# Kernel tuning notes

Measured on AMD Instinct MI355X. Metric: run time of the kernel, lower is better.

Reference implementation:

```python
import jax, jax.numpy as jnp
import numpy as np

B, SEQ, C, H, OVERLAP, G, K, D = 16, 8192, 192, 16, 4, 6, 1024, 8
FIX = H * C                      # 3072 (proj_ratio = 1.0, no in/out proj)
DG = (FIX * OVERLAP) // G        # 2048, per-group dim
W = SEQ // H                     # 512 time frames
T = W // OVERLAP                 # 128 grouped frames


def _l2norm(x, eps=1e-12):
    return x / jnp.clip(jnp.linalg.norm(x, axis=-1, keepdims=True), eps)


def setup_inputs() -> dict:
    key = jax.random.key(0)
    k0, k1, k2, k3 = jax.random.split(key, 4)
    z = jax.random.normal(k0, (B, SEQ, C), jnp.float32)
    # stacked per-group parameters (all groups have equal dim DG)
    proj_down = jax.random.normal(k1, (G, DG, D), jnp.float32) * (DG ** -0.5)
    proj_up = jax.random.normal(k2, (G, D, DG), jnp.float32) * (D ** -0.5)
    codebooks = jax.random.normal(k3, (G, K, D), jnp.float32)
    return {"z": z, "proj_down": proj_down, "proj_up": proj_up, "codebooks": codebooks}


def reference(z, proj_down, proj_up, codebooks):
    # --- pre_process: 'b (h w) c -> b w (c h)' then fold overlap ---
    zz = z.reshape(B, H, W, C)                      # b h w c
    zz = jnp.transpose(zz, (0, 2, 3, 1))            # b w c h
    zz = zz.reshape(B, W, FIX)                      # b w (c h)
    zz = zz.reshape(B, T, OVERLAP * FIX)            # fold overlap frames
    zg = zz.reshape(B, T, G, DG)                    # split into G groups

    # --- per-group codebook VQ (vectorized over G) ---
    z_e = jnp.einsum('btgd,gde->btge', zg, proj_down)           # (B,T,G,D)
    sim = jnp.einsum('btge,gke->btgk', _l2norm(z_e), _l2norm(codebooks))
    code = jnp.argmax(sim, axis=-1)                             # (B,T,G)
    gidx = jnp.arange(G)[None, None, :]
    z_q = codebooks[gidx, code]                                 # (B,T,G,D)

    # per-batch-element losses, mean over (T, D) per group, averaged over groups
    commitment = jnp.mean((z_e - jax.lax.stop_gradient(z_q)) ** 2, axis=(1, 3)).mean(axis=1)
    codebook_l = jnp.mean((jax.lax.stop_gradient(z_e) - z_q) ** 2, axis=(1, 3)).mean(axis=1)

    # straight-through estimator + up projection
    z_q_st = z_e + jax.lax.stop_gradient(z_q - z_e)
    z_up = jnp.einsum('btge,ged->btgd', z_q_st, proj_up)        # (B,T,G,DG)
    z_up = z_up.reshape(B, T, OVERLAP * FIX)

    # --- post_process: unfold overlap, 'b w (c h) -> b (h w) c' ---
    out = z_up.reshape(B, W, FIX)                   # b w (c h)
    out = out.reshape(B, W, C, H)
    out = jnp.transpose(out, (0, 3, 1, 2))          # b h w c
    out = out.reshape(B, SEQ, C)
    return out, commitment, codebook_l
```

## Files before the change

### kernel.cpp

```cpp
#include <hip/hip_runtime.h>
#include <math.h>

#define B_ 16
#define SEQ_ 8192
#define C_ 192
#define H_ 16
#define OV_ 4
#define G_ 6
#define K_ 1024
#define D_ 8
#define DG_ 2048
#define W_ 512
#define T_ 128
#define TT 4
#define OUT_ELEMS (B_ * SEQ_ * C_)



__global__ __launch_bounds__(256) void vq_prep(
    const float* __restrict__ pd, const float* __restrict__ pu,
    const float* __restrict__ cb,
    float* __restrict__ pd_p, float* __restrict__ pu_p,
    double* __restrict__ cbn, float* __restrict__ loss_slots)
{
  int i = blockIdx.x * 256 + threadIdx.x;
  if (i < 98304) {
    int e = i & 7, dp = (i >> 3) & 2047, g = i >> 14;
    int h = dp >> 7, ul = dp & 127, d = (ul << 4) + h;
    pd_p[i] = pd[(g << 14) + (d << 3) + e];
  } else if (i < 196608) {
    int i2 = i - 98304;
    int dp = i2 & 2047, e = (i2 >> 11) & 7, g = i2 >> 14;
    int h = dp >> 7, ul = dp & 127, d = (ul << 4) + h;
    pu_p[i2] = pu[(g << 14) + (e << 11) + d];
  } else if (i < 202752) {
    int j = i - 196608;
    const float* row = cb + (j << 3);
    double ss = 0.0;
    #pragma unroll
    for (int e = 0; e < 8; ++e) { double x = (double)row[e]; ss += x * x; }
    double inv = 1.0 / fmax(sqrt(ss), 1e-12);
    #pragma unroll
    for (int e = 0; e < 8; ++e) cbn[(j << 3) + e] = (double)row[e] * inv;
  } else if (i < 202784) {
    loss_slots[i - 202752] = 0.0f;
  }
}

__global__ __launch_bounds__(256) void vq_main(
    const float* __restrict__ z, const float* __restrict__ cb,
    const float* __restrict__ pd_p, const float* __restrict__ pu_p,
    const double* __restrict__ cbn,
    float* __restrict__ out, float* __restrict__ loss_slots)
{
  __shared__ __align__(16) float zs[TT * DG_];
  __shared__ double ze_d[TT * 8];
  __shared__ float  zq_s[TT * 8];
  __shared__ double wr_s[4][TT];
  __shared__ int    wr_k[4][TT];
  __shared__ float  lossv[TT];

  const int tid = threadIdx.x;
  const int tc  = blockIdx.x;
  const int g   = blockIdx.y;
  const int b   = blockIdx.z;

  const float* zb = z + (size_t)b * (SEQ_ * C_);

  #pragma unroll
  for (int t = 0; t < TT; ++t) {
    int wbase = (tc * TT + t) * OV_;
    #pragma unroll
    for (int j = 0; j < 2; ++j) {
      int v  = j * 256 + tid;
      int h  = v >> 5;
      int ul = (v & 31) << 2;
      int u  = (g << 7) + ul;
      int o  = (u * 683) >> 17;
      int c  = u - o * 192;
      const float4 val = *(const float4*)(zb + (h * 512 + wbase + o) * 192 + c);
      *(float4*)(&zs[t * DG_ + (h << 7) + ul]) = val;
    }
  }
  __syncthreads();

  double acc[TT][8];
  #pragma unroll
  for (int t = 0; t < TT; ++t)
    #pragma unroll
    for (int e = 0; e < 8; ++e) acc[t][e] = 0.0;

  #pragma unroll
  for (int i = 0; i < 8; ++i) {
    int dp = i * 256 + tid;
    const float4 p0 = *(const float4*)(pd_p + ((((g << 11) + dp) << 3)));
    const float4 p1 = *(const float4*)(pd_p + ((((g << 11) + dp) << 3) + 4));
    #pragma unroll
    for (int t = 0; t < TT; ++t) {
      double zv = (double)zs[t * DG_ + dp];
      acc[t][0] = fma(zv, (double)p0.x, acc[t][0]);
      acc[t][1] = fma(zv, (double)p0.y, acc[t][1]);
      acc[t][2] = fma(zv, (double)p0.z, acc[t][2]);
      acc[t][3] = fma(zv, (double)p0.w, acc[t][3]);
      acc[t][4] = fma(zv, (double)p1.x, acc[t][4]);
      acc[t][5] = fma(zv, (double)p1.y, acc[t][5]);
      acc[t][6] = fma(zv, (double)p1.z, acc[t][6]);
      acc[t][7] = fma(zv, (double)p1.w, acc[t][7]);
    }
  }

  double* part_d = (double*)zs;
  #pragma unroll
  for (int r = 0; r < 2; ++r) {
    __syncthreads();
    #pragma unroll
    for (int kkl = 0; kkl < 16; ++kkl) {
      int kk = r * 16 + kkl;
      part_d[kkl * 256 + tid] = acc[kk >> 3][kk & 7];
    }
    __syncthreads();
    int kkl = tid >> 4, jj = tid & 15;
    double partial = 0.0;
    #pragma unroll
    for (int s = 0; s < 16; ++s) {
      int p = (s + tid) & 15;
      partial += part_d[kkl * 256 + jj * 16 + p];
    }
    partial += __shfl_down(partial, 8);
    partial += __shfl_down(partial, 4);
    partial += __shfl_down(partial, 2);
    partial += __shfl_down(partial, 1);
    if (jj == 0) ze_d[r * 16 + kkl] = partial;
  }
  __syncthreads();

  double cd[4][8];
  #pragma unroll
  for (int q = 0; q < 4; ++q) {
    const double* cr = cbn + (((g << 10) + (q << 8) + tid) << 3);
    #pragma unroll
    for (int e = 0; e < 8; ++e) cd[q][e] = cr[e];
  }
  double bs[TT]; int bk[TT];
  #pragma unroll
  for (int t = 0; t < TT; ++t) {
    double zr[8];
    #pragma unroll
    for (int e = 0; e < 8; ++e) zr[e] = ze_d[t * 8 + e];
    bs[t] = -1.0e300; bk[t] = 0x7fffffff;
    #pragma unroll
    for (int q = 0; q < 4; ++q) {
      double s = 0.0;
      #pragma unroll
      for (int e = 0; e < 8; ++e) s = fma(zr[e], cd[q][e], s);
      int k = (q << 8) + tid;
      if (s > bs[t]) { bs[t] = s; bk[t] = k; }
    }
  }
  #pragma unroll
  for (int m = 32; m >= 1; m >>= 1) {
    #pragma unroll
    for (int t = 0; t < TT; ++t) {
      double os = __shfl_xor(bs[t], m);
      int    ok = __shfl_xor(bk[t], m);
      if (os > bs[t] || (os == bs[t] && ok < bk[t])) { bs[t] = os; bk[t] = ok; }
    }
  }
  int wv = tid >> 6;
  if ((tid & 63) == 0) {
    #pragma unroll
    for (int t = 0; t < TT; ++t) { wr_s[wv][t] = bs[t]; wr_k[wv][t] = bk[t]; }
  }
  __syncthreads();
  if (tid < TT) {
    int t = tid;
    double s0 = wr_s[0][t]; int k0 = wr_k[0][t];
    #pragma unroll
    for (int w2 = 1; w2 < 4; ++w2) {
      double s1 = wr_s[w2][t]; int k1 = wr_k[w2][t];
      if (s1 > s0 || (s1 == s0 && k1 < k0)) { s0 = s1; k0 = k1; }
    }
    const float* crow = cb + (((g << 10) + k0) << 3);
    double l = 0.0;
    #pragma unroll
    for (int e = 0; e < 8; ++e) {
      float qv = crow[e];
      zq_s[t * 8 + e] = qv;
      double dd = ze_d[t * 8 + e] - (double)qv;
      l = fma(dd, dd, l);
    }
    lossv[t] = (float)l;
  }
  __syncthreads();
  if (tid == 0) {
    float l = (lossv[0] + lossv[1] + lossv[2] + lossv[3]) * (1.0f / (T_ * D_ * G_));
    atomicAdd(loss_slots + b, l);
    atomicAdd(loss_slots + 16 + b, l);
  }

  float zqr[TT][8];
  #pragma unroll
  for (int t = 0; t < TT; ++t)
    #pragma unroll
    for (int e = 0; e < 8; ++e) zqr[t][e] = zq_s[t * 8 + e];

  #pragma unroll
  for (int j = 0; j < 8; ++j) {
    int dp = j * 256 + tid;
    int h = dp >> 7, ul = dp & 127;
    int u = (g << 7) + ul;
    int o = (u * 683) >> 17;
    int c = u - o * 192;
    float pv[8];
    #pragma unroll
    for (int e = 0; e < 8; ++e) pv[e] = pu_p[(g << 14) + (e << 11) + dp];
    size_t base = ((size_t)(b * SEQ_) + h * 512 + tc * (TT * OV_) + o) * 192 + c;
    #pragma unroll
    for (int t = 0; t < TT; ++t) {
      float v = 0.f;
      #pragma unroll
      for (int e = 0; e < 8; ++e) v = fmaf(zqr[t][e], pv[e], v);
      out[base + (size_t)(t * OV_ * 192)] = v;
    }
  }
}

extern "C" void kernel_launch(void* const* d_in, const int* in_sizes, int n_in,
                              void* d_out, int out_size, void* d_ws, size_t ws_size,
                              hipStream_t stream)
{
  const float* z  = (const float*)d_in[0];
  const float* pd = (const float*)d_in[1];
  const float* pu = (const float*)d_in[2];
  const float* cb = (const float*)d_in[3];
  float* out = (float*)d_out;
  float* loss_slots = out + OUT_ELEMS;

  float*  pd_p = (float*)d_ws;
  float*  pu_p = pd_p + 98304;
  double* cbn  = (double*)(pu_p + 98304);

  vq_prep<<<793, 256, 0, stream>>>(pd, pu, cb, pd_p, pu_p, cbn, loss_slots);
  dim3 grid(T_ / TT, G_, B_);
  vq_main<<<grid, 256, 0, stream>>>(z, cb, pd_p, pu_p, cbn, out, loss_slots);
}
```

Before: 212.4 us.

## Compute down-projection per wavefront directly from global memory, dropping shared staging

The down-projection no longer stages four time frames of z (32 KB) in shared memory followed by a two-pass shared-memory reduction. Each wavefront now owns one time frame, reads z and proj_down straight from global memory, and reduces its eight accumulators with xor shuffles. This cuts the per-block LDS footprint and several barriers, and a launch-bounds hint of 6 blocks per CU is added to raise occupancy. In exchange, each block reads proj_down four times instead of once, relying on cache, and the z reads become strided float2 loads rather than float4.

```diff
diff --git a/kernel.cpp b/kernel.cpp
--- a/kernel.cpp
+++ b/kernel.cpp
@@ -47,90 +47,72 @@
   }
 }
 
-__global__ __launch_bounds__(256) void vq_main(
+__global__ __launch_bounds__(256, 6) void vq_main(
     const float* __restrict__ z, const float* __restrict__ cb,
     const float* __restrict__ pd_p, const float* __restrict__ pu_p,
     const double* __restrict__ cbn,
     float* __restrict__ out, float* __restrict__ loss_slots)
 {
-  __shared__ __align__(16) float zs[TT * DG_];
   __shared__ double ze_d[TT * 8];
   __shared__ float  zq_s[TT * 8];
   __shared__ double wr_s[4][TT];
   __shared__ int    wr_k[4][TT];
   __shared__ float  lossv[TT];
 
-  const int tid = threadIdx.x;
-  const int tc  = blockIdx.x;
-  const int g   = blockIdx.y;
-  const int b   = blockIdx.z;
+  const int tid  = threadIdx.x;
+  const int lane = tid & 63;
+  const int wv   = tid >> 6;
+  const int tc   = blockIdx.x;
+  const int g    = blockIdx.y;
+  const int b    = blockIdx.z;
 
   const float* zb = z + (size_t)b * (SEQ_ * C_);
 
-  #pragma unroll
-  for (int t = 0; t < TT; ++t) {
-    int wbase = (tc * TT + t) * OV_;
-    #pragma unroll
-    for (int j = 0; j < 2; ++j) {
-      int v  = j * 256 + tid;
-      int h  = v >> 5;
-      int ul = (v & 31) << 2;
-      int u  = (g << 7) + ul;
-      int o  = (u * 683) >> 17;
-      int c  = u - o * 192;
-      const float4 val = *(const float4*)(zb + (h * 512 + wbase + o) * 192 + c);
-      *(float4*)(&zs[t * DG_ + (h << 7) + ul]) = val;
-    }
-  }
-  __syncthreads();
-
-  double acc[TT][8];
-  #pragma unroll
-  for (int t = 0; t < TT; ++t)
-    #pragma unroll
-    for (int e = 0; e < 8; ++e) acc[t][e] = 0.0;
-
-  #pragma unroll
-  for (int i = 0; i < 8; ++i) {
-    int dp = i * 256 + tid;
-    const float4 p0 = *(const float4*)(pd_p + ((((g << 11) + dp) << 3)));
-    const float4 p1 = *(const float4*)(pd_p + ((((g << 11) + dp) << 3) + 4));
-    #pragma unroll
-    for (int t = 0; t < TT; ++t) {
-      double zv = (double)zs[t * DG_ + dp];
-      acc[t][0] = fma(zv, (double)p0.x, acc[t][0]);
-      acc[t][1] = fma(zv, (double)p0.y, acc[t][1]);
-      acc[t][2] = fma(zv, (double)p0.z, acc[t][2]);
-      acc[t][3] = fma(zv, (double)p0.w, acc[t][3]);
-      acc[t][4] = fma(zv, (double)p1.x, acc[t][4]);
-      acc[t][5] = fma(zv, (double)p1.y, acc[t][5]);
-      acc[t][6] = fma(zv, (double)p1.z, acc[t][6]);
-      acc[t][7] = fma(zv, (double)p1.w, acc[t][7]);
-    }
-  }
-
-  double* part_d = (double*)zs;
-  #pragma unroll
-  for (int r = 0; r < 2; ++r) {
-    __syncthreads();
-    #pragma unroll
-    for (int kkl = 0; kkl < 16; ++kkl) {
-      int kk = r * 16 + kkl;
-      part_d[kkl * 256 + tid] = acc[kk >> 3][kk & 7];
-    }
-    __syncthreads();
-    int kkl = tid >> 4, jj = tid & 15;
-    double partial = 0.0;
-    #pragma unroll
-    for (int s = 0; s < 16; ++s) {
-      int p = (s + tid) & 15;
-      partial += part_d[kkl * 256 + jj * 16 + p];
-    }
-    partial += __shfl_down(partial, 8);
-    partial += __shfl_down(partial, 4);
-    partial += __shfl_down(partial, 2);
-    partial += __shfl_down(partial, 1);
-    if (jj == 0) ze_d[r * 16 + kkl] = partial;
+  {
+    const int wbase = (tc * TT + wv) * OV_;
+    const float* zcol = zb + (size_t)wbase * 192 + (g << 7) + (lane << 1);
+    const float4* pdg = (const float4*)(pd_p + ((g << 11) << 3));
+
+    double acc[8];
+    #pragma unroll
+    for (int e = 0; e < 8; ++e) acc[e] = 0.0;
+
+    #pragma unroll 2
+    for (int h = 0; h < 16; ++h) {
+      const float2 zv = *(const float2*)(zcol + h * (512 * 192));
+      const int dp = (h << 7) + (lane << 1);
+      const float4 p00 = pdg[(dp << 1) + 0];
+      const float4 p01 = pdg[(dp << 1) + 1];
+      const float4 p10 = pdg[(dp << 1) + 2];
+      const float4 p11 = pdg[(dp << 1) + 3];
+      const double z0 = (double)zv.x, z1 = (double)zv.y;
+      acc[0] = fma(z0, (double)p00.x, acc[0]);
+      acc[1] = fma(z0, (double)p00.y, acc[1]);
+      acc[2] = fma(z0, (double)p00.z, acc[2]);
+      acc[3] = fma(z0, (double)p00.w, acc[3]);
+      acc[4] = fma(z0, (double)p01.x, acc[4]);
+      acc[5] = fma(z0, (double)p01.y, acc[5]);
+      acc[6] = fma(z0, (double)p01.z, acc[6]);
+      acc[7] = fma(z0, (double)p01.w, acc[7]);
+      acc[0] = fma(z1, (double)p10.x, acc[0]);
+      acc[1] = fma(z1, (double)p10.y, acc[1]);
+      acc[2] = fma(z1, (double)p10.z, acc[2]);
+      acc[3] = fma(z1, (double)p10.w, acc[3]);
+      acc[4] = fma(z1, (double)p11.x, acc[4]);
+      acc[5] = fma(z1, (double)p11.y, acc[5]);
+      acc[6] = fma(z1, (double)p11.z, acc[6]);
+      acc[7] = fma(z1, (double)p11.w, acc[7]);
+    }
+
+    #pragma unroll
+    for (int m = 32; m >= 1; m >>= 1) {
+      #pragma unroll
+      for (int e = 0; e < 8; ++e) acc[e] += __shfl_xor(acc[e], m);
+    }
+    if (lane == 0) {
+      #pragma unroll
+      for (int e = 0; e < 8; ++e) ze_d[wv * 8 + e] = acc[e];
+    }
   }
   __syncthreads();
 
@@ -166,10 +148,10 @@
       if (os > bs[t] || (os == bs[t] && ok < bk[t])) { bs[t] = os; bk[t] = ok; }
     }
   }
-  int wv = tid >> 6;
+  int wv4 = tid >> 6;
   if ((tid & 63) == 0) {
     #pragma unroll
-    for (int t = 0; t < TT; ++t) { wr_s[wv][t] = bs[t]; wr_k[wv][t] = bk[t]; }
+    for (int t = 0; t < TT; ++t) { wr_s[wv4][t] = bs[t]; wr_k[wv4][t] = bk[t]; }
   }
   __syncthreads();
   if (tid < TT) {
```

Result: slower. 372.2 us (+75.3%).

## Stream z directly from global into projection, split output dims across half-blocks

Applied to the files above, without the earlier changes.

The down-projection no longer stages a 32 KB tile of z in shared memory. Each thread now reads float2 pairs of z straight from global memory, and the two halves of the block each handle 4 of the 8 output dims. This halves the register accumulators and shrinks shared memory to a small reduction buffer, and launch bounds now request 6 blocks per CU. The aim is higher occupancy and no LDS staging or barrier cost. The codebook scoring loop is also reorganised to load two codebook rows at a time, which lowers register pressure. The trade-off is less coalesced global loads of z, which are 8-byte strided per thread, and each z element is now read twice, once by each half-block.

```diff
diff --git a/kernel.cpp b/kernel.cpp
--- a/kernel.cpp
+++ b/kernel.cpp
@@ -47,13 +47,13 @@
   }
 }
 
-__global__ __launch_bounds__(256) void vq_main(
+__global__ __launch_bounds__(256, 6) void vq_main(
     const float* __restrict__ z, const float* __restrict__ cb,
     const float* __restrict__ pd_p, const float* __restrict__ pu_p,
     const double* __restrict__ cbn,
     float* __restrict__ out, float* __restrict__ loss_slots)
 {
-  __shared__ __align__(16) float zs[TT * DG_];
+  __shared__ double part_d[16 * 128];
   __shared__ double ze_d[TT * 8];
   __shared__ float  zq_s[TT * 8];
   __shared__ double wr_s[4][TT];
@@ -61,100 +61,100 @@
   __shared__ float  lossv[TT];
 
   const int tid = threadIdx.x;
+  const int tl  = tid & 127;
+  const int eh  = tid >> 7;
   const int tc  = blockIdx.x;
   const int g   = blockIdx.y;
   const int b   = blockIdx.z;
 
   const float* zb = z + (size_t)b * (SEQ_ * C_);
 
-  #pragma unroll
-  for (int t = 0; t < TT; ++t) {
-    int wbase = (tc * TT + t) * OV_;
-    #pragma unroll
-    for (int j = 0; j < 2; ++j) {
-      int v  = j * 256 + tid;
-      int h  = v >> 5;
-      int ul = (v & 31) << 2;
-      int u  = (g << 7) + ul;
-      int o  = (u * 683) >> 17;
-      int c  = u - o * 192;
-      const float4 val = *(const float4*)(zb + (h * 512 + wbase + o) * 192 + c);
-      *(float4*)(&zs[t * DG_ + (h << 7) + ul]) = val;
-    }
-  }
-  __syncthreads();
-
-  double acc[TT][8];
+  double acc[TT][4];
   #pragma unroll
   for (int t = 0; t < TT; ++t)
     #pragma unroll
-    for (int e = 0; e < 8; ++e) acc[t][e] = 0.0;
-
-  #pragma unroll
-  for (int i = 0; i < 8; ++i) {
-    int dp = i * 256 + tid;
-    const float4 p0 = *(const float4*)(pd_p + ((((g << 11) + dp) << 3)));
-    const float4 p1 = *(const float4*)(pd_p + ((((g << 11) + dp) << 3) + 4));
-    #pragma unroll
-    for (int t = 0; t < TT; ++t) {
-      double zv = (double)zs[t * DG_ + dp];
-      acc[t][0] = fma(zv, (double)p0.x, acc[t][0]);
-      acc[t][1] = fma(zv, (double)p0.y, acc[t][1]);
-      acc[t][2] = fma(zv, (double)p0.z, acc[t][2]);
-      acc[t][3] = fma(zv, (double)p0.w, acc[t][3]);
-      acc[t][4] = fma(zv, (double)p1.x, acc[t][4]);
-      acc[t][5] = fma(zv, (double)p1.y, acc[t][5]);
-      acc[t][6] = fma(zv, (double)p1.z, acc[t][6]);
-      acc[t][7] = fma(zv, (double)p1.w, acc[t][7]);
-    }
-  }
-
-  double* part_d = (double*)zs;
+    for (int j = 0; j < 4; ++j) acc[t][j] = 0.0;
+
+  {
+    const int hofs = tl >> 6;
+    const int ul2  = (tl & 63) << 1;
+    const float* zbase = zb + (size_t)(tc * (TT * OV_)) * 192 + (g << 7) + ul2;
+    const float* pdg = pd_p + ((g << 11) << 3) + (eh << 2);
+
+    #pragma unroll 2
+    for (int i = 0; i < 8; ++i) {
+      const int h = (i << 1) + hofs;
+      const float* zp = zbase + (size_t)h * (512 * 192);
+      float2 zv[TT];
+      #pragma unroll
+      for (int t = 0; t < TT; ++t)
+        zv[t] = *(const float2*)(zp + t * (OV_ * 192));
+      const int dp0 = (i << 8) + (tl << 1);
+      const float4 pa = *(const float4*)(pdg + (dp0 << 3));
+      const float4 pb = *(const float4*)(pdg + ((dp0 + 1) << 3));
+      #pragma unroll
+      for (int t = 0; t < TT; ++t) {
+        const double z0 = (double)zv[t].x, z1 = (double)zv[t].y;
+        acc[t][0] = fma(z0, (double)pa.x, acc[t][0]);
+        acc[t][1] = fma(z0, (double)pa.y, acc[t][1]);
+        acc[t][2] = fma(z0, (double)pa.z, acc[t][2]);
+        acc[t][3] = fma(z0, (double)pa.w, acc[t][3]);
+        acc[t][0] = fma(z1, (double)pb.x, acc[t][0]);
+        acc[t][1] = fma(z1, (double)pb.y, acc[t][1]);
+        acc[t][2] = fma(z1, (double)pb.z, acc[t][2]);
+        acc[t][3] = fma(z1, (double)pb.w, acc[t][3]);
+      }
+    }
+  }
+
   #pragma unroll
   for (int r = 0; r < 2; ++r) {
     __syncthreads();
     #pragma unroll
-    for (int kkl = 0; kkl < 16; ++kkl) {
-      int kk = r * 16 + kkl;
-      part_d[kkl * 256 + tid] = acc[kk >> 3][kk & 7];
-    }
+    for (int tl2 = 0; tl2 < 2; ++tl2)
+      #pragma unroll
+      for (int j = 0; j < 4; ++j)
+        part_d[(((tl2 << 3) + (eh << 2) + j) << 7) + tl] = acc[(r << 1) + tl2][j];
     __syncthreads();
-    int kkl = tid >> 4, jj = tid & 15;
+    const int slot = tid >> 4, jj = tid & 15;
     double partial = 0.0;
     #pragma unroll
-    for (int s = 0; s < 16; ++s) {
-      int p = (s + tid) & 15;
-      partial += part_d[kkl * 256 + jj * 16 + p];
-    }
-    partial += __shfl_down(partial, 8);
-    partial += __shfl_down(partial, 4);
-    partial += __shfl_down(partial, 2);
-    partial += __shfl_down(partial, 1);
-    if (jj == 0) ze_d[r * 16 + kkl] = partial;
+    for (int s = 0; s < 8; ++s)
+      partial += part_d[(slot << 7) + (s << 4) + jj];
+    partial += __shfl_down(partial, 8, 16);
+    partial += __shfl_down(partial, 4, 16);
+    partial += __shfl_down(partial, 2, 16);
+    partial += __shfl_down(partial, 1, 16);
+    if (jj == 0) ze_d[(r << 4) + slot] = partial;
   }
   __syncthreads();
 
-  double cd[4][8];
-  #pragma unroll
-  for (int q = 0; q < 4; ++q) {
-    const double* cr = cbn + (((g << 10) + (q << 8) + tid) << 3);
-    #pragma unroll
-    for (int e = 0; e < 8; ++e) cd[q][e] = cr[e];
-  }
   double bs[TT]; int bk[TT];
   #pragma unroll
-  for (int t = 0; t < TT; ++t) {
-    double zr[8];
-    #pragma unroll
-    for (int e = 0; e < 8; ++e) zr[e] = ze_d[t * 8 + e];
-    bs[t] = -1.0e300; bk[t] = 0x7fffffff;
-    #pragma unroll
-    for (int q = 0; q < 4; ++q) {
-      double s = 0.0;
-      #pragma unroll
-      for (int e = 0; e < 8; ++e) s = fma(zr[e], cd[q][e], s);
-      int k = (q << 8) + tid;
-      if (s > bs[t]) { bs[t] = s; bk[t] = k; }
+  for (int t = 0; t < TT; ++t) { bs[t] = -1.0e300; bk[t] = 0x7fffffff; }
+
+  #pragma unroll
+  for (int qp = 0; qp < 2; ++qp) {
+    double cd2[2][8];
+    #pragma unroll
+    for (int qi = 0; qi < 2; ++qi) {
+      const double* cr = cbn + (((g << 10) + (((qp << 1) + qi) << 8) + tid) << 3);
+      #pragma unroll
+      for (int e = 0; e < 8; ++e) cd2[qi][e] = cr[e];
+    }
+    #pragma unroll
+    for (int t = 0; t < TT; ++t) {
+      double s0 = 0.0, s1 = 0.0;
+      #pragma unroll
+      for (int e = 0; e < 8; ++e) {
+        const double zr = ze_d[t * 8 + e];
+        s0 = fma(zr, cd2[0][e], s0);
+        s1 = fma(zr, cd2[1][e], s1);
+      }
+      const int k0 = ((qp << 1) << 8) + tid;
+      const int k1 = (((qp << 1) + 1) << 8) + tid;
+      if (s0 > bs[t]) { bs[t] = s0; bk[t] = k0; }
+      if (s1 > bs[t]) { bs[t] = s1; bk[t] = k1; }
     }
   }
   #pragma unroll
@@ -166,10 +166,10 @@
       if (os > bs[t] || (os == bs[t] && ok < bk[t])) { bs[t] = os; bk[t] = ok; }
     }
   }
-  int wv = tid >> 6;
+  const int wv4 = tid >> 6;
   if ((tid & 63) == 0) {
     #pragma unroll
-    for (int t = 0; t < TT; ++t) { wr_s[wv][t] = bs[t]; wr_k[wv][t] = bk[t]; }
+    for (int t = 0; t < TT; ++t) { wr_s[wv4][t] = bs[t]; wr_k[wv4][t] = bk[t]; }
   }
   __syncthreads();
   if (tid < TT) {
```

Result: slower. 342.5 us (+61.3%).

## Process two time chunks per block with register prefetch of next z tile

Applied to the files above, without the earlier changes.

Each block now handles two consecutive time chunks instead of one, halving the grid. While the first chunk's projection runs, the second chunk's z tile is loaded into registers, then written to shared memory after the reduction finishes. The goal is to hide global load latency behind compute. The cost is more register pressure from the 8 float4 prefetch registers and fewer blocks (1536) available to fill the GPU.

```diff
diff --git a/kernel.cpp b/kernel.cpp
--- a/kernel.cpp
+++ b/kernel.cpp
@@ -61,7 +61,7 @@
   __shared__ float  lossv[TT];
 
   const int tid = threadIdx.x;
-  const int tc  = blockIdx.x;
+  const int bx  = blockIdx.x;
   const int g   = blockIdx.y;
   const int b   = blockIdx.z;
 
@@ -69,7 +69,7 @@
 
   #pragma unroll
   for (int t = 0; t < TT; ++t) {
-    int wbase = (tc * TT + t) * OV_;
+    int wbase = ((bx << 1) * TT + t) * OV_;
     #pragma unroll
     for (int j = 0; j < 2; ++j) {
       int v  = j * 256 + tid;
@@ -84,143 +84,180 @@
   }
   __syncthreads();
 
-  double acc[TT][8];
+  float4 zpref[8];
+
   #pragma unroll
-  for (int t = 0; t < TT; ++t)
-    #pragma unroll
-    for (int e = 0; e < 8; ++e) acc[t][e] = 0.0;
-
-  #pragma unroll
-  for (int i = 0; i < 8; ++i) {
-    int dp = i * 256 + tid;
-    const float4 p0 = *(const float4*)(pd_p + ((((g << 11) + dp) << 3)));
-    const float4 p1 = *(const float4*)(pd_p + ((((g << 11) + dp) << 3) + 4));
+  for (int cc = 0; cc < 2; ++cc) {
+    const int tcc = (bx << 1) + cc;
+
+    if (cc == 0) {
+      #pragma unroll
+      for (int t = 0; t < TT; ++t) {
+        int wbase = (((bx << 1) + 1) * TT + t) * OV_;
+        #pragma unroll
+        for (int j = 0; j < 2; ++j) {
+          int v  = j * 256 + tid;
+          int h  = v >> 5;
+          int ul = (v & 31) << 2;
+          int u  = (g << 7) + ul;
+          int o  = (u * 683) >> 17;
+          int c  = u - o * 192;
+          zpref[t * 2 + j] = *(const float4*)(zb + (h * 512 + wbase + o) * 192 + c);
+        }
+      }
+    }
+
+    double acc[TT][8];
+    #pragma unroll
+    for (int t = 0; t < TT; ++t)
+      #pragma unroll
+      for (int e = 0; e < 8; ++e) acc[t][e] = 0.0;
+
+    #pragma unroll
+    for (int i = 0; i < 8; ++i) {
+      int dp = i * 256 + tid;
+      const float4 p0 = *(const float4*)(pd_p + ((((g << 11) + dp) << 3)));
+      const float4 p1 = *(const float4*)(pd_p + ((((g << 11) + dp) << 3) + 4));
+      #pragma unroll
+      for (int t = 0; t < TT; ++t) {
+        double zv = (double)zs[t * DG_ + dp];
+        acc[t][0] = fma(zv, (double)p0.x, acc[t][0]);
+        acc[t][1] = fma(zv, (double)p0.y, acc[t][1]);
+        acc[t][2] = fma(zv, (double)p0.z, acc[t][2]);
+        acc[t][3] = fma(zv, (double)p0.w, acc[t][3]);
+        acc[t][4] = fma(zv, (double)p1.x, acc[t][4]);
+        acc[t][5] = fma(zv, (double)p1.y, acc[t][5]);
+        acc[t][6] = fma(zv, (double)p1.z, acc[t][6]);
+        acc[t][7] = fma(zv, (double)p1.w, acc[t][7]);
+      }
+    }
+
+    double* part_d = (double*)zs;
+    #pragma unroll
+    for (int r = 0; r < 2; ++r) {
+      __syncthreads();
+      #pragma unroll
+      for (int kkl = 0; kkl < 16; ++kkl) {
+        int kk = r * 16 + kkl;
+        part_d[kkl * 256 + tid] = acc[kk >> 3][kk & 7];
+      }
+      __syncthreads();
+      int kkl = tid >> 4, jj = tid & 15;
+      double partial = 0.0;
+      #pragma unroll
+      for (int s = 0; s < 16; ++s) {
+        int p = (s + tid) & 15;
+        partial += part_d[kkl * 256 + jj * 16 + p];
+      }
+      partial += __shfl_down(partial, 8);
+      partial += __shfl_down(partial, 4);
+      partial += __shfl_down(partial, 2);
+      partial += __shfl_down(partial, 1);
+      if (jj == 0) ze_d[r * 16 + kkl] = partial;
+    }
+    __syncthreads();
+
+    if (cc == 0) {
+      #pragma unroll
+      for (int t = 0; t < TT; ++t) {
+        #pragma unroll
+        for (int j = 0; j < 2; ++j) {
+          int v  = j * 256 + tid;
+          int h  = v >> 5;
+          int ul = (v & 31) << 2;
+          *(float4*)(&zs[t * DG_ + (h << 7) + ul]) = zpref[t * 2 + j];
+        }
+      }
+    }
+
+    double cd[4][8];
+    #pragma unroll
+    for (int q = 0; q < 4; ++q) {
+      const double* cr = cbn + (((g << 10) + (q << 8) + tid) << 3);
+      #pragma unroll
+      for (int e = 0; e < 8; ++e) cd[q][e] = cr[e];
+    }
+    double bs[TT]; int bk[TT];
     #pragma unroll
     for (int t = 0; t < TT; ++t) {
-      double zv = (double)zs[t * DG_ + dp];
-      acc[t][0] = fma(zv, (double)p0.x, acc[t][0]);
-      acc[t][1] = fma(zv, (double)p0.y, acc[t][1]);
-      acc[t][2] = fma(zv, (double)p0.z, acc[t][2]);
-      acc[t][3] = fma(zv, (double)p0.w, acc[t][3]);
-      acc[t][4] = fma(zv, (double)p1.x, acc[t][4]);
-      acc[t][5] = fma(zv, (double)p1.y, acc[t][5]);
-      acc[t][6] = fma(zv, (double)p1.z, acc[t][6]);
-      acc[t][7] = fma(zv, (double)p1.w, acc[t][7]);
-    }
-  }
-
-  double* part_d = (double*)zs;
-  #pragma unroll
-  for (int r = 0; r < 2; ++r) {
+      double zr[8];
+      #pragma unroll
+      for (int e = 0; e < 8; ++e) zr[e] = ze_d[t * 8 + e];
+      bs[t] = -1.0e300; bk[t] = 0x7fffffff;
+      #pragma unroll
+      for (int q = 0; q < 4; ++q) {
+        double s = 0.0;
+        #pragma unroll
+        for (int e = 0; e < 8; ++e) s = fma(zr[e], cd[q][e], s);
+        int k = (q << 8) + tid;
+        if (s > bs[t]) { bs[t] = s; bk[t] = k; }
+      }
+    }
+    #pragma unroll
+    for (int m = 32; m >= 1; m >>= 1) {
+      #pragma unroll
+      for (int t = 0; t < TT; ++t) {
+        double os = __shfl_xor(bs[t], m);
+        int    ok = __shfl_xor(bk[t], m);
+        if (os > bs[t] || (os == bs[t] && ok < bk[t])) { bs[t] = os; bk[t] = ok; }
+      }
+    }
+    int wv = tid >> 6;
+    if ((tid & 63) == 0) {
+      #pragma unroll
+      for (int t = 0; t < TT; ++t) { wr_s[wv][t] = bs[t]; wr_k[wv][t] = bk[t]; }
+    }
     __syncthreads();
-    #pragma unroll
-    for (int kkl = 0; kkl < 16; ++kkl) {
-      int kk = r * 16 + kkl;
-      part_d[kkl * 256 + tid] = acc[kk >> 3][kk & 7];
+    if (tid < TT) {
+      int t = tid;
+      double s0 = wr_s[0][t]; int k0 = wr_k[0][t];
+      #pragma unroll
+      for (int w2 = 1; w2 < 4; ++w2) {
+        double s1 = wr_s[w2][t]; int k1 = wr_k[w2][t];
+        if (s1 > s0 || (s1 == s0 && k1 < k0)) { s0 = s1; k0 = k1; }
+      }
+      const float* crow = cb + (((g << 10) + k0) << 3);
+      double l = 0.0;
+      #pragma unroll
+      for (int e = 0; e < 8; ++e) {
+        float qv = crow[e];
+        zq_s[t * 8 + e] = qv;
+        double dd = ze_d[t * 8 + e] - (double)qv;
+        l = fma(dd, dd, l);
+      }
+      lossv[t] = (float)l;
     }
     __syncthreads();
-    int kkl = tid >> 4, jj = tid & 15;
-    double partial = 0.0;
-    #pragma unroll
-    for (int s = 0; s < 16; ++s) {
-      int p = (s + tid) & 15;
-      partial += part_d[kkl * 256 + jj * 16 + p];
-    }
-    partial += __shfl_down(partial, 8);
-    partial += __shfl_down(partial, 4);
-    partial += __shfl_down(partial, 2);
-    partial += __shfl_down(partial, 1);
-    if (jj == 0) ze_d[r * 16 + kkl] = partial;
-  }
-  __syncthreads();
-
-  double cd[4][8];
-  #pragma unroll
-  for (int q = 0; q < 4; ++q) {
-    const double* cr = cbn + (((g << 10) + (q << 8) + tid) << 3);
-    #pragma unroll
-    for (int e = 0; e < 8; ++e) cd[q][e] = cr[e];
-  }
-  double bs[TT]; int bk[TT];
-  #pragma unroll
-  for (int t = 0; t < TT; ++t) {
-    double zr[8];
-    #pragma unroll
-    for (int e = 0; e < 8; ++e) zr[e] = ze_d[t * 8 + e];
-    bs[t] = -1.0e300; bk[t] = 0x7fffffff;
-    #pragma unroll
-    for (int q = 0; q < 4; ++q) {
-      double s = 0.0;
-      #pragma unroll
-      for (int e = 0; e < 8; ++e) s = fma(zr[e], cd[q][e], s);
-      int k = (q << 8) + tid;
-      if (s > bs[t]) { bs[t] = s; bk[t] = k; }
-    }
-  }
-  #pragma unroll
-  for (int m = 32; m >= 1; m >>= 1) {
-    #pragma unroll
-    for (int t = 0; t < TT; ++t) {
-      double os = __shfl_xor(bs[t], m);
-      int    ok = __shfl_xor(bk[t], m);
-      if (os > bs[t] || (os == bs[t] && ok < bk[t])) { bs[t] = os; bk[t] = ok; }
-    }
-  }
-  int wv = tid >> 6;
-  if ((tid & 63) == 0) {
-    #pragma unroll
-    for (int t = 0; t < TT; ++t) { wr_s[wv][t] = bs[t]; wr_k[wv][t] = bk[t]; }
-  }
-  __syncthreads();
-  if (tid < TT) {
-    int t = tid;
-    double s0 = wr_s[0][t]; int k0 = wr_k[0][t];
-    #pragma unroll
-    for (int w2 = 1; w2 < 4; ++w2) {
-      double s1 = wr_s[w2][t]; int k1 = wr_k[w2][t];
-      if (s1 > s0 || (s1 == s0 && k1 < k0)) { s0 = s1; k0 = k1; }
-    }
-    const float* crow = cb + (((g << 10) + k0) << 3);
-    double l = 0.0;
-    #pragma unroll
-    for (int e = 0; e < 8; ++e) {
-      float qv = crow[e];
-      zq_s[t * 8 + e] = qv;
-      double dd = ze_d[t * 8 + e] - (double)qv;
-      l = fma(dd, dd, l);
-    }
-    lossv[t] = (float)l;
-  }
-  __syncthreads();
-  if (tid == 0) {
-    float l = (lossv[0] + lossv[1] + lossv[2] + lossv[3]) * (1.0f / (T_ * D_ * G_));
-    atomicAdd(loss_slots + b, l);
-    atomicAdd(loss_slots + 16 + b, l);
-  }
-
-  float zqr[TT][8];
-  #pragma unroll
-  for (int t = 0; t < TT; ++t)
-    #pragma unroll
-    for (int e = 0; e < 8; ++e) zqr[t][e] = zq_s[t * 8 + e];
-
-  #pragma unroll
-  for (int j = 0; j < 8; ++j) {
-    int dp = j * 256 + tid;
-    int h = dp >> 7, ul = dp & 127;
-    int u = (g << 7) + ul;
-    int o = (u * 683) >> 17;
-    int c = u - o * 192;
-    float pv[8];
-    #pragma unroll
-    for (int e = 0; e < 8; ++e) pv[e] = pu_p[(g << 14) + (e << 11) + dp];
-    size_t base = ((size_t)(b * SEQ_) + h * 512 + tc * (TT * OV_) + o) * 192 + c;
-    #pragma unroll
-    for (int t = 0; t < TT; ++t) {
-      float v = 0.f;
-      #pragma unroll
-      for (int e = 0; e < 8; ++e) v = fmaf(zqr[t][e], pv[e], v);
-      out[base + (size_t)(t * OV_ * 192)] = v;
+    if (tid == 0) {
+      float l = (lossv[0] + lossv[1] + lossv[2] + lossv[3]) * (1.0f / (T_ * D_ * G_));
+      atomicAdd(loss_slots + b, l);
+      atomicAdd(loss_slots + 16 + b, l);
+    }
+
+    float zqr[TT][8];
+    #pragma unroll
+    for (int t = 0; t < TT; ++t)
+      #pragma unroll
+      for (int e = 0; e < 8; ++e) zqr[t][e] = zq_s[t * 8 + e];
+
+    #pragma unroll
+    for (int j = 0; j < 8; ++j) {
+      int dp = j * 256 + tid;
+      int h = dp >> 7, ul = dp & 127;
+      int u = (g << 7) + ul;
+      int o = (u * 683) >> 17;
+      int c = u - o * 192;
+      float pv[8];
+      #pragma unroll
+      for (int e = 0; e < 8; ++e) pv[e] = pu_p[(g << 14) + (e << 11) + dp];
+      size_t base = ((size_t)(b * SEQ_) + h * 512 + tcc * (TT * OV_) + o) * 192 + c;
+      #pragma unroll
+      for (int t = 0; t < TT; ++t) {
+        float v = 0.f;
+        #pragma unroll
+        for (int e = 0; e < 8; ++e) v = fmaf(zqr[t][e], pv[e], v);
+        out[base + (size_t)(t * OV_ * 192)] = v;
+      }
     }
   }
 }
@@ -241,6 +278,6 @@
   double* cbn  = (double*)(pu_p + 98304);
 
   vq_prep<<<793, 256, 0, stream>>>(pd, pu, cb, pd_p, pu_p, cbn, loss_slots);
-  dim3 grid(T_ / TT, G_, B_);
+  dim3 grid(T_ / TT / 2, G_, B_);
   vq_main<<<grid, 256, 0, stream>>>(z, cb, pd_p, pu_p, cbn, out, loss_slots);
 }
```

Result: slower. 238.4 us (+12.3%).
